# Performance work log

Hardware: AMD Instinct MI355X
Metric: run time of the kernel (lower is better)

## Reference

```python
import jax, jax.numpy as jnp
import numpy as np

D_MODEL = 1024  # scale uses sqrt(d_model), matching the source's sqrt(C)

def setup_inputs() -> dict:
    key = jax.random.key(0)
    kx, kq, kk, kv = jax.random.split(key, 4)
    B, T, C, H = 8, 2048, D_MODEL, 64
    s = 1.0 / np.sqrt(C)
    return {
        "x": jax.random.normal(kx, (B, T, C), dtype=jnp.float32),
        "Wq": jax.random.normal(kq, (C, H), dtype=jnp.float32) * s,
        "Wk": jax.random.normal(kk, (C, H), dtype=jnp.float32) * s,
        "Wv": jax.random.normal(kv, (C, H), dtype=jnp.float32) * s,
    }

def reference(x, Wq, Wk, Wv):
    B, T, C = x.shape
    q = jnp.einsum("btc,ch->bth", x, Wq)
    k = jnp.einsum("btc,ch->bth", x, Wk)
    v = jnp.einsum("btc,ch->bth", x, Wv)
    # scores scaled by 1/sqrt(C) (C = d_model), faithful to source
    wei = jnp.einsum("bth,bsh->bts", q, k) / jnp.sqrt(jnp.float32(C))
    causal = jnp.tril(jnp.ones((T, T), dtype=bool))  # [T, T]
    wei = jnp.where(causal, wei, -jnp.inf)
    wei = jax.nn.softmax(wei, axis=-1)
    out = jnp.einsum("bts,bsh->bth", wei, v)
    return out
```

## Files before the change

kernel.cpp:

```cpp
#include <hip/hip_runtime.h>

typedef unsigned short u16;
typedef __attribute__((ext_vector_type(4))) float f32x4;
typedef __attribute__((ext_vector_type(8))) short bf16x8;
typedef __attribute__((ext_vector_type(4))) u16 u16x4;
typedef __attribute__((ext_vector_type(8))) u16 u16x8;

#define MFMA(a, b, c) __builtin_amdgcn_mfma_f32_16x16x32_bf16(a, b, c, 0, 0, 0)

__device__ __forceinline__ u16 f2bf(float f) {
    unsigned u = __float_as_uint(f);
    u += 0x7fffu + ((u >> 16) & 1u);
    return (u16)(u >> 16);
}
__device__ __forceinline__ float bf2f(u16 h) {
    unsigned u = ((unsigned)h) << 16;
    return __uint_as_float(u);
}

__device__ __forceinline__ void load_lds16(const void* g, void* l) {
    __builtin_amdgcn_global_load_lds((const __attribute__((address_space(1))) void*)g,
                                     (__attribute__((address_space(3))) void*)l,
                                     16, 0, 0);
}

__global__ void wt_pack(const float* __restrict__ Wq, const float* __restrict__ Wk,
                        const float* __restrict__ Wv, u16* __restrict__ Wtt) {
    const int k = blockIdx.x;
    const int n = threadIdx.x;
    const float* W = (n < 64) ? Wq : (n < 128 ? Wk : Wv);
    const float v = W[(size_t)k * 64 + (n & 63)];
    const int kt = k >> 6, ks = k & 63, c = ks >> 3, ci = ks & 7;
    Wtt[(size_t)kt * 12288 + n * 64 + (((c ^ (n & 7)) << 3) + ci)] = f2bf(v);
}

__global__ __launch_bounds__(256, 2) void qkv_gemm(const float* __restrict__ x,
                                                   const u16* __restrict__ Wtt,
                                                   u16* __restrict__ qo,
                                                   u16* __restrict__ ko,
                                                   u16* __restrict__ vT) {
    const int tid = threadIdx.x;
    const int lane = tid & 63, wave = tid >> 6;
    const int lr = lane & 15, lg = lane >> 4;
    const int m0 = blockIdx.x * 32;

    __shared__ __align__(16) float xs[2][32 * 64];
    __shared__ __align__(16) u16 ws[2][192 * 64];

    f32x4 acc[2][3];
#pragma unroll
    for (int m = 0; m < 2; ++m)
#pragma unroll
        for (int n = 0; n < 3; ++n) acc[m][n] = (f32x4){0.f, 0.f, 0.f, 0.f};

    const int srow = tid >> 4;
    const int schk = tid & 15;

    {
#pragma unroll
        for (int j = 0; j < 2; ++j) {
            const int rr = j * 16 + srow;
            const float* src = x + (size_t)(m0 + rr) * 1024 + ((schk ^ (rr & 7)) << 2);
            load_lds16(src, &xs[0][j * 1024 + wave * 256]);
        }
#pragma unroll
        for (int j = 0; j < 6; ++j) {
            const u16* src = Wtt + (size_t)j * 2048 + tid * 8;
            load_lds16(src, &ws[0][j * 2048 + wave * 512]);
        }
    }
    __syncthreads();

    for (int kt = 0; kt < 16; ++kt) {
        const int cur = kt & 1;
        if (kt < 15) {
            const int nxt = cur ^ 1;
#pragma unroll
            for (int j = 0; j < 2; ++j) {
                const int rr = j * 16 + srow;
                const float* src =
                    x + (size_t)(m0 + rr) * 1024 + (kt + 1) * 64 + ((schk ^ (rr & 7)) << 2);
                load_lds16(src, &xs[nxt][j * 1024 + wave * 256]);
            }
#pragma unroll
            for (int j = 0; j < 6; ++j) {
                const u16* src = Wtt + (size_t)(kt + 1) * 12288 + j * 2048 + tid * 8;
                load_lds16(src, &ws[nxt][j * 2048 + wave * 512]);
            }
        }
#pragma unroll
        for (int h = 0; h < 2; ++h) {
            bf16x8 a[2];
#pragma unroll
            for (int mm = 0; mm < 2; ++mm) {
                const int rr = mm * 16 + lr;
                const int c0 = h * 8 + lg * 2;
                f32x4 f0 = *(const f32x4*)&xs[cur][rr * 64 + ((c0 ^ (rr & 7)) << 2)];
                f32x4 f1 = *(const f32x4*)&xs[cur][rr * 64 + (((c0 + 1) ^ (rr & 7)) << 2)];
                bf16x8 t;
#pragma unroll
                for (int i = 0; i < 4; ++i) {
                    t[i] = (short)f2bf(f0[i]);
                    t[i + 4] = (short)f2bf(f1[i]);
                }
                a[mm] = t;
            }
#pragma unroll
            for (int nl = 0; nl < 3; ++nl) {
                const int row = (wave * 3 + nl) * 16 + lr;
                const int cb = h * 4 + lg;
                const bf16x8 b = *(const bf16x8*)&ws[cur][row * 64 + ((cb ^ (row & 7)) << 3)];
                acc[0][nl] = MFMA(a[0], b, acc[0][nl]);
                acc[1][nl] = MFMA(a[1], b, acc[1][nl]);
            }
        }
        __syncthreads();
    }

    const float SCQ = 0.0450842200277801f;
    const int bb = m0 >> 11;
    const int tb = m0 & 2047;
#pragma unroll
    for (int mm = 0; mm < 2; ++mm)
#pragma unroll
        for (int nl = 0; nl < 3; ++nl) {
            const int col = (wave * 3 + nl) * 16 + lr;
            const int rl = mm * 16 + lg * 4;
            if (col < 64) {
#pragma unroll
                for (int r = 0; r < 4; ++r)
                    qo[(size_t)(m0 + rl + r) * 64 + col] = f2bf(acc[mm][nl][r] * SCQ);
            } else if (col < 128) {
#pragma unroll
                for (int r = 0; r < 4; ++r)
                    ko[(size_t)(m0 + rl + r) * 64 + (col - 64)] = f2bf(acc[mm][nl][r]);
            } else {
                u16x4 pk;
#pragma unroll
                for (int r = 0; r < 4; ++r) pk[r] = f2bf(acc[mm][nl][r]);
                *(u16x4*)&vT[(size_t)(bb * 64 + (col - 128)) * 2048 + tb + rl] = pk;
            }
        }
}

#define PPITCH 72
__global__ __launch_bounds__(256, 3) void attn_part(const u16* __restrict__ q,
                                                    const u16* __restrict__ k,
                                                    const u16* __restrict__ vT,
                                                    u16* __restrict__ Opb,
                                                    float* __restrict__ Lp) {
    const int b = blockIdx.x & 7;
    int g = blockIdx.x >> 3;
    int qt = 31, rem = g;
    while (rem >= (qt >> 3) + 1) { rem -= (qt >> 3) + 1; --qt; }
    const int c0 = rem;
    const int q0 = qt * 64;
    const int kv_lo = c0 * 512;
    const int kv_hi = min(kv_lo + 512, q0 + 64);
    const int ntiles = (kv_hi - kv_lo) >> 6;
    const int slot = (b * 32 + qt) * 4 + c0;

    __shared__ __align__(16) u16 lK[2][64 * 64];
    __shared__ __align__(16) u16 lV[2][64 * 64];
    __shared__ __align__(16) u16 lP[4][16 * PPITCH];

    const int tid = threadIdx.x;
    const int wave = tid >> 6, lane = tid & 63;
    const int lr = lane & 15, lg = lane >> 4;

    const u16* qb = q + (size_t)b * 2048 * 64;
    const u16* kb = k + (size_t)b * 2048 * 64;
    const u16* vb = vT + (size_t)b * 64 * 2048;

    const int myrow = q0 + wave * 16 + lr;
    const bf16x8 qf0 = *(const bf16x8*)(qb + (size_t)myrow * 64 + lg * 8);
    const bf16x8 qf1 = *(const bf16x8*)(qb + (size_t)myrow * 64 + 32 + lg * 8);

    f32x4 oacc[4];
#pragma unroll
    for (int n = 0; n < 4; ++n) oacc[n] = (f32x4){0.f, 0.f, 0.f, 0.f};
    float rs = 0.f;

#define ASTAGE(bufi, kv0_)                                                             \
    {                                                                                  \
        _Pragma("unroll") for (int j = 0; j < 2; ++j) {                                \
            const int cid = j * 256 + wave * 64 + lane;                                \
            const int row = cid >> 3, cc = cid & 7;                                    \
            load_lds16(kb + (size_t)((kv0_) + row) * 64 + ((cc ^ (row & 7)) << 3),     \
                       &lK[bufi][(j * 256 + wave * 64) * 8]);                          \
            load_lds16(vb + (size_t)row * 2048 + (kv0_) + ((cc ^ (row & 7)) << 3),     \
                       &lV[bufi][(j * 256 + wave * 64) * 8]);                          \
        }                                                                              \
    }

    ASTAGE(0, kv_lo);
    __syncthreads();

    for (int it = 0; it < ntiles; ++it) {
        const int cur = it & 1;
        if (it + 1 < ntiles) ASTAGE(cur ^ 1, kv_lo + (it + 1) * 64);

        const int kv0 = kv_lo + it * 64;
        if (kv0 <= q0 + wave * 16 + 15) {
            f32x4 s[4];
#pragma unroll
            for (int n = 0; n < 4; ++n) {
                const int row = n * 16 + lr;
                const bf16x8 kf0 = *(const bf16x8*)&lK[cur][row * 64 + ((lg ^ (row & 7)) << 3)];
                const bf16x8 kf1 =
                    *(const bf16x8*)&lK[cur][row * 64 + (((4 + lg) ^ (row & 7)) << 3)];
                f32x4 a = (f32x4){0.f, 0.f, 0.f, 0.f};
                a = MFMA(kf0, qf0, a);
                a = MFMA(kf1, qf1, a);
                s[n] = a;
            }

            const bool msk = (kv0 + 63 > q0 + wave * 16);
#pragma unroll
            for (int n = 0; n < 4; ++n) {
                u16x4 pk;
#pragma unroll
                for (int r = 0; r < 4; ++r) {
                    const int kvi = kv0 + n * 16 + lg * 4 + r;
                    const float p = (!msk || kvi <= myrow) ? exp2f(s[n][r]) : 0.f;
                    rs += p;
                    pk[r] = f2bf(p);
                }
                *(u16x4*)&lP[wave][lr * PPITCH + n * 16 + lg * 4] = pk;
            }

#pragma unroll
            for (int kc = 0; kc < 2; ++kc) {
                const bf16x8 pf = *(const bf16x8*)&lP[wave][lr * PPITCH + kc * 32 + lg * 8];
#pragma unroll
                for (int n = 0; n < 4; ++n) {
                    const int row = n * 16 + lr;
                    const bf16x8 vf =
                        *(const bf16x8*)&lV[cur][row * 64 + (((kc * 4 + lg) ^ (row & 7)) << 3)];
                    oacc[n] = MFMA(pf, vf, oacc[n]);
                }
            }
        }
        __syncthreads();
    }

    rs += __shfl_xor(rs, 16);
    rs += __shfl_xor(rs, 32);
    if (lane < 16) Lp[slot * 64 + wave * 16 + lr] = rs;

    u16* op = Opb + (size_t)slot * 4096 + wave * 1024;
#pragma unroll
    for (int n = 0; n < 4; ++n)
#pragma unroll
        for (int r = 0; r < 4; ++r)
            op[n * 256 + (lg * 4 + r) * 16 + lr] = f2bf(oacc[n][r]);
}

__global__ __launch_bounds__(256) void attn_combine(const u16* __restrict__ Opb,
                                                    const float* __restrict__ Lp,
                                                    float* __restrict__ out) {
    const int gid = blockIdx.x * 256 + threadIdx.x;
    const int colg = gid & 7;
    const int row = gid >> 3;
    const int b = row >> 11, tt = row & 2047;
    const int qt = tt >> 6, i = tt & 63;
    const int nc = (qt >> 3) + 1;
    const size_t sbase = (size_t)(b * 32 + qt) * 4;
    const int sub0 = (i >> 4) * 1024 + (colg >> 1) * 256 + (i & 15) * 16 + (colg & 1) * 8;

    float O[8] = {0.f, 0.f, 0.f, 0.f, 0.f, 0.f, 0.f, 0.f};
    float L = 0.f;
    for (int c = 0; c < nc; ++c) {
        const u16x8 v = *(const u16x8*)&Opb[(sbase + c) * 4096 + sub0];
#pragma unroll
        for (int j = 0; j < 8; ++j) O[j] += bf2f(v[j]);
        L += Lp[(sbase + c) * 64 + i];
    }
    const float rinv = 1.0f / L;
    f32x4 o0, o1;
#pragma unroll
    for (int j = 0; j < 4; ++j) {
        o0[j] = O[j] * rinv;
        o1[j] = O[4 + j] * rinv;
    }
    float* ob = out + (size_t)row * 64 + colg * 8;
    *(f32x4*)(ob) = o0;
    *(f32x4*)(ob + 4) = o1;
}

extern "C" void kernel_launch(void* const* d_in, const int* in_sizes, int n_in,
                              void* d_out, int out_size, void* d_ws, size_t ws_size,
                              hipStream_t stream) {
    const float* x = (const float*)d_in[0];
    const float* Wq = (const float*)d_in[1];
    const float* Wk = (const float*)d_in[2];
    const float* Wv = (const float*)d_in[3];
    float* out = (float*)d_out;

    char* ws = (char*)d_ws;
    u16* Wtt = (u16*)ws;
    u16* qb = (u16*)(ws + (512 << 10));
    u16* kb = (u16*)(ws + (512 << 10) + (2 << 20));
    u16* vT = (u16*)(ws + (512 << 10) + (4 << 20));
    u16* Opb = (u16*)(ws + (8 << 20));
    float* Lp = (float*)(ws + (20 << 20));

    wt_pack<<<1024, 192, 0, stream>>>(Wq, Wk, Wv, Wtt);
    qkv_gemm<<<512, 256, 0, stream>>>(x, Wtt, qb, kb, vT);
    attn_part<<<640, 256, 0, stream>>>(qb, kb, vT, Opb, Lp);
    attn_combine<<<512, 256, 0, stream>>>(Opb, Lp, out);
}
```

Measured before the change: 54.99 us.

## Halve QKV GEMM K-tile for higher occupancy and raise MFMA priority in attention

The QKV projection GEMM now stages K-tiles of 32 instead of 64. This halves the LDS footprint per block, and launch bounds are raised to 4 blocks per CU so more blocks can be resident to hide load latency. The weight packing layout and swizzle are changed to match the narrower tile. The trade-off is twice as many loop iterations and barriers. Separately, the attention kernel brackets its MFMA sections with s_setprio so matrix work from different waves can interleave with the softmax work.

```diff
diff --git a/kernel.cpp b/kernel.cpp
--- a/kernel.cpp
+++ b/kernel.cpp
@@ -30,11 +30,11 @@
     const int n = threadIdx.x;
     const float* W = (n < 64) ? Wq : (n < 128 ? Wk : Wv);
     const float v = W[(size_t)k * 64 + (n & 63)];
-    const int kt = k >> 6, ks = k & 63, c = ks >> 3, ci = ks & 7;
-    Wtt[(size_t)kt * 12288 + n * 64 + (((c ^ (n & 7)) << 3) + ci)] = f2bf(v);
-}
-
-__global__ __launch_bounds__(256, 2) void qkv_gemm(const float* __restrict__ x,
+    const int kt = k >> 5, ks = k & 31, c = ks >> 3, ci = ks & 7;
+    Wtt[(size_t)kt * 6144 + n * 32 + (((c ^ (n & 3)) << 3) + ci)] = f2bf(v);
+}
+
+__global__ __launch_bounds__(256, 4) void qkv_gemm(const float* __restrict__ x,
                                                    const u16* __restrict__ Wtt,
                                                    u16* __restrict__ qo,
                                                    u16* __restrict__ ko,
@@ -44,8 +44,8 @@
     const int lr = lane & 15, lg = lane >> 4;
     const int m0 = blockIdx.x * 32;
 
-    __shared__ __align__(16) float xs[2][32 * 64];
-    __shared__ __align__(16) u16 ws[2][192 * 64];
+    __shared__ __align__(16) float xs[2][32 * 32];
+    __shared__ __align__(16) u16 ws[2][192 * 32];
 
     f32x4 acc[2][3];
 #pragma unroll
@@ -53,66 +53,46 @@
 #pragma unroll
         for (int n = 0; n < 3; ++n) acc[m][n] = (f32x4){0.f, 0.f, 0.f, 0.f};
 
-    const int srow = tid >> 4;
-    const int schk = tid & 15;
-
-    {
-#pragma unroll
-        for (int j = 0; j < 2; ++j) {
-            const int rr = j * 16 + srow;
-            const float* src = x + (size_t)(m0 + rr) * 1024 + ((schk ^ (rr & 7)) << 2);
-            load_lds16(src, &xs[0][j * 1024 + wave * 256]);
-        }
-#pragma unroll
-        for (int j = 0; j < 6; ++j) {
-            const u16* src = Wtt + (size_t)j * 2048 + tid * 8;
-            load_lds16(src, &ws[0][j * 2048 + wave * 512]);
-        }
-    }
+    const int xrow = tid >> 3, xc = tid & 7;
+
+#define QSTAGE(bufi, kt_)                                                              \
+    {                                                                                  \
+        load_lds16(x + (size_t)(m0 + xrow) * 1024 + (kt_)*32 + ((xc ^ (xrow & 7)) << 2), \
+                   &xs[bufi][wave * 256]);                                             \
+        _Pragma("unroll") for (int j = 0; j < 3; ++j) {                                \
+            load_lds16(Wtt + (size_t)(kt_)*6144 + (j * 256 + tid) * 8,                 \
+                       &ws[bufi][(j * 256 + wave * 64) * 8]);                          \
+        }                                                                              \
+    }
+
+    QSTAGE(0, 0);
     __syncthreads();
 
-    for (int kt = 0; kt < 16; ++kt) {
+    for (int kt = 0; kt < 32; ++kt) {
         const int cur = kt & 1;
-        if (kt < 15) {
-            const int nxt = cur ^ 1;
-#pragma unroll
-            for (int j = 0; j < 2; ++j) {
-                const int rr = j * 16 + srow;
-                const float* src =
-                    x + (size_t)(m0 + rr) * 1024 + (kt + 1) * 64 + ((schk ^ (rr & 7)) << 2);
-                load_lds16(src, &xs[nxt][j * 1024 + wave * 256]);
-            }
-#pragma unroll
-            for (int j = 0; j < 6; ++j) {
-                const u16* src = Wtt + (size_t)(kt + 1) * 12288 + j * 2048 + tid * 8;
-                load_lds16(src, &ws[nxt][j * 2048 + wave * 512]);
-            }
-        }
-#pragma unroll
-        for (int h = 0; h < 2; ++h) {
-            bf16x8 a[2];
-#pragma unroll
-            for (int mm = 0; mm < 2; ++mm) {
-                const int rr = mm * 16 + lr;
-                const int c0 = h * 8 + lg * 2;
-                f32x4 f0 = *(const f32x4*)&xs[cur][rr * 64 + ((c0 ^ (rr & 7)) << 2)];
-                f32x4 f1 = *(const f32x4*)&xs[cur][rr * 64 + (((c0 + 1) ^ (rr & 7)) << 2)];
-                bf16x8 t;
-#pragma unroll
-                for (int i = 0; i < 4; ++i) {
-                    t[i] = (short)f2bf(f0[i]);
-                    t[i + 4] = (short)f2bf(f1[i]);
-                }
-                a[mm] = t;
-            }
-#pragma unroll
-            for (int nl = 0; nl < 3; ++nl) {
-                const int row = (wave * 3 + nl) * 16 + lr;
-                const int cb = h * 4 + lg;
-                const bf16x8 b = *(const bf16x8*)&ws[cur][row * 64 + ((cb ^ (row & 7)) << 3)];
-                acc[0][nl] = MFMA(a[0], b, acc[0][nl]);
-                acc[1][nl] = MFMA(a[1], b, acc[1][nl]);
-            }
+        if (kt < 31) QSTAGE(cur ^ 1, kt + 1);
+
+        bf16x8 a[2];
+#pragma unroll
+        for (int mm = 0; mm < 2; ++mm) {
+            const int rr = mm * 16 + lr;
+            const int g0 = lg * 2;
+            f32x4 f0 = *(const f32x4*)&xs[cur][rr * 32 + ((g0 ^ (rr & 7)) << 2)];
+            f32x4 f1 = *(const f32x4*)&xs[cur][rr * 32 + (((g0 + 1) ^ (rr & 7)) << 2)];
+            bf16x8 t;
+#pragma unroll
+            for (int i = 0; i < 4; ++i) {
+                t[i] = (short)f2bf(f0[i]);
+                t[i + 4] = (short)f2bf(f1[i]);
+            }
+            a[mm] = t;
+        }
+#pragma unroll
+        for (int nl = 0; nl < 3; ++nl) {
+            const int row = (wave * 3 + nl) * 16 + lr;
+            const bf16x8 b = *(const bf16x8*)&ws[cur][row * 32 + ((lg ^ (row & 3)) << 3)];
+            acc[0][nl] = MFMA(a[0], b, acc[0][nl]);
+            acc[1][nl] = MFMA(a[1], b, acc[1][nl]);
         }
         __syncthreads();
     }
@@ -203,6 +183,7 @@
         const int kv0 = kv_lo + it * 64;
         if (kv0 <= q0 + wave * 16 + 15) {
             f32x4 s[4];
+            __builtin_amdgcn_s_setprio(1);
 #pragma unroll
             for (int n = 0; n < 4; ++n) {
                 const int row = n * 16 + lr;
@@ -214,6 +195,7 @@
                 a = MFMA(kf1, qf1, a);
                 s[n] = a;
             }
+            __builtin_amdgcn_s_setprio(0);
 
             const bool msk = (kv0 + 63 > q0 + wave * 16);
 #pragma unroll
@@ -229,6 +211,7 @@
                 *(u16x4*)&lP[wave][lr * PPITCH + n * 16 + lg * 4] = pk;
             }
 
+            __builtin_amdgcn_s_setprio(1);
 #pragma unroll
             for (int kc = 0; kc < 2; ++kc) {
                 const bf16x8 pf = *(const bf16x8*)&lP[wave][lr * PPITCH + kc * 32 + lg * 8];
@@ -240,6 +223,7 @@
                     oacc[n] = MFMA(pf, vf, oacc[n]);
                 }
             }
+            __builtin_amdgcn_s_setprio(0);
         }
         __syncthreads();
     }
```

After: 56.28 us. 1.02x slower.
